# Performance work log

Measured on AMD Instinct MI355X. Metric: run time of the kernel, lower is better.

The kernel has to match this reference:

```python
import jax, jax.numpy as jnp
import numpy as np

N_ROWS = 262144
FEAT = 1024
N_CORES = 4096
SEG = N_ROWS // N_CORES
H1 = H2 = H3 = 1024
NUM_CLASSES = 2
BN_EPS = 1e-5


def setup_inputs() -> dict:
    key = jax.random.key(0)
    ks = jax.random.split(key, 12)
    x = jax.random.normal(ks[0], (N_ROWS, FEAT), dtype=jnp.float32)
    # equal-length segments: start indices 0, SEG, 2*SEG, ...
    corelen = (jnp.arange(N_CORES) * SEG).astype(jnp.int64)
    def lin(k, din, dout):
        kw, kb = jax.random.split(k)
        W = jax.random.normal(kw, (din, dout), dtype=jnp.float32) / np.sqrt(din)
        b = jnp.zeros((dout,), dtype=jnp.float32)
        return W, b
    W1, b1 = lin(ks[1], FEAT, H1)
    W2, b2 = lin(ks[2], H1, H2)
    W3, b3 = lin(ks[3], H2, H3)
    W4, b4 = lin(ks[4], H3, NUM_CLASSES)
    g1 = jnp.ones((H1,), jnp.float32); be1 = jnp.zeros((H1,), jnp.float32)
    g2 = jnp.ones((H2,), jnp.float32); be2 = jnp.zeros((H2,), jnp.float32)
    g3 = jnp.ones((H3,), jnp.float32); be3 = jnp.zeros((H3,), jnp.float32)
    return {"x": x, "corelen": corelen,
            "W1": W1, "b1": b1, "g1": g1, "be1": be1,
            "W2": W2, "b2": b2, "g2": g2, "be2": be2,
            "W3": W3, "b3": b3, "g3": g3, "be3": be3,
            "W4": W4, "b4": b4}


def _batchnorm(h, g, b):
    # BatchNorm1d, training mode: biased batch statistics over the batch dim
    m = jnp.mean(h, axis=0)
    v = jnp.mean(jnp.square(h - m), axis=0)
    return g * (h - m) * jax.lax.rsqrt(v + BN_EPS) + b


def reference(x, corelen, W1, b1, g1, be1, W2, b2, g2, be2, W3, b3, g3, be3, W4, b4):
    n = x.shape[0]
    # segment id of row r = number of starts <= r, minus 1 (rows before
    # corelen[0] get id -1 and are dropped, matching the torch loop)
    seg_ids = jnp.searchsorted(corelen, jnp.arange(n), side="right") - 1
    agg = jax.ops.segment_sum(x, seg_ids, num_segments=corelen.shape[0])  # [C, FEAT]
    h = jax.nn.relu(_batchnorm(agg @ W1 + b1, g1, be1))
    h = jax.nn.relu(_batchnorm(h @ W2 + b2, g2, be2))
    h = jax.nn.relu(_batchnorm(h @ W3 + b3, g3, be3))
    return h @ W4 + b4  # [C, NUM_CLASSES]
```

## Files before the change

### kernel.cpp

```cpp
#include <hip/hip_runtime.h>
#include <hip/hip_bf16.h>
#include <stdint.h>

#define N_ROWS 262144
#define FEAT 1024
#define N_CORES 4096
#define HDIM 1024
#define BN_EPS 1e-5f

typedef __attribute__((ext_vector_type(8))) short bf16x8;
typedef __attribute__((ext_vector_type(8))) unsigned short u16x8;
typedef __attribute__((ext_vector_type(4))) float f32x4;

__device__ __forceinline__ unsigned short f2bf(float f) {
  __hip_bfloat16 h = __float2bfloat16(f);
  return __builtin_bit_cast(unsigned short, h);
}
__device__ __forceinline__ float bf2f(unsigned short u) {
  unsigned int x = ((unsigned int)u) << 16;
  return __builtin_bit_cast(float, x);
}

__device__ __forceinline__ void gll16(const unsigned short* g, unsigned short* l) {
  __builtin_amdgcn_global_load_lds(
      (const __attribute__((address_space(1))) void*)g,
      (__attribute__((address_space(3))) void*)l, 16, 0, 0);
}

__global__ __launch_bounds__(256)
void k_prep(const float* __restrict__ x, const int* __restrict__ corelen,
            unsigned short* __restrict__ aggb,
            const float* __restrict__ W1, const float* __restrict__ W2,
            const float* __restrict__ W3, unsigned short* __restrict__ Wt,
            float* __restrict__ stats) {
  const int bid = blockIdx.x;
  const int t = threadIdx.x;
  if (bid < N_CORES) {
    const int seg = bid;
    const int start = corelen[seg];
    const int end = (seg + 1 < N_CORES) ? corelen[seg + 1] : N_ROWS;
    f32x4 a0 = {0.f, 0.f, 0.f, 0.f};
    f32x4 a1 = {0.f, 0.f, 0.f, 0.f};
    f32x4 a2 = {0.f, 0.f, 0.f, 0.f};
    f32x4 a3 = {0.f, 0.f, 0.f, 0.f};
    const f32x4* xp = (const f32x4*)(x + (size_t)start * FEAT) + t;
    int r = start;
    for (; r + 4 <= end; r += 4) {
      const f32x4 v0 = __builtin_nontemporal_load(xp);
      const f32x4 v1 = __builtin_nontemporal_load(xp + 256);
      const f32x4 v2 = __builtin_nontemporal_load(xp + 512);
      const f32x4 v3 = __builtin_nontemporal_load(xp + 768);
      a0 += v0; a1 += v1; a2 += v2; a3 += v3;
      xp += 4 * 256;
    }
    for (; r < end; ++r) {
      a0 += *xp;
      xp += 256;
    }
    a0 += a1; a2 += a3; a0 += a2;
    ushort4 o;
    o.x = f2bf(a0.x); o.y = f2bf(a0.y); o.z = f2bf(a0.z); o.w = f2bf(a0.w);
    *(ushort4*)(aggb + (size_t)seg * FEAT + t * 4) = o;
  } else if (bid < N_CORES + 3 * 1024) {
    __shared__ unsigned short tile[32][33];
    const int id = bid - N_CORES;
    const int l = id >> 10;
    const int q = id & 1023;
    const int n0 = (q & 31) * 32;
    const int k0 = (q >> 5) * 32;
    const float* W = (l == 0) ? W1 : (l == 1) ? W2 : W3;
    unsigned short* Wo = Wt + (size_t)l * HDIM * HDIM;
    const int tx = t & 31, ty = t >> 5;
#pragma unroll
    for (int i = 0; i < 4; ++i)
      tile[ty + 8 * i][tx] = f2bf(W[(size_t)(k0 + ty + 8 * i) * HDIM + n0 + tx]);
    __syncthreads();
#pragma unroll
    for (int i = 0; i < 4; ++i)
      Wo[(size_t)(n0 + ty + 8 * i) * HDIM + k0 + tx] = tile[tx][ty + 8 * i];
  } else {
#pragma unroll
    for (int i = 0; i < 24; ++i) stats[t + i * 256] = 0.f;
  }
}

#define BM 64
#define BN 64
#define BK 64
#define NT (HDIM / BK)
__global__ __launch_bounds__(64)
void k_gemm_bt(const unsigned short* __restrict__ A,
               const unsigned short* __restrict__ Bt,
               const float* __restrict__ bias,
               unsigned short* __restrict__ C,
               float* __restrict__ sums, float* __restrict__ sumsq) {
  __shared__ unsigned short As[2][BM * BK];
  __shared__ unsigned short Bs[2][BN * BK];
  const int lane = threadIdx.x;
  const int tileM = blockIdx.x * BM;
  const int tileN = blockIdx.y * BN;
  const int fr = lane & 15;
  const int kk = (lane >> 4) * 8;
  const int lr = lane >> 3;
  const int sc = ((lane & 7) * 8) ^ (lr << 3);

  const unsigned short* pA = A + (size_t)(tileM + lr) * HDIM + sc;
  const unsigned short* pB = Bt + (size_t)(tileN + lr) * HDIM + sc;

  f32x4 acc[4][4] = {};

#define STAGE(buf, k0)                                                     \
  do {                                                                     \
    _Pragma("unroll") for (int j = 0; j < 8; ++j)                          \
        gll16(pA + (k0) + j * 8 * HDIM, &As[buf][(j * 8) * BK]);           \
    _Pragma("unroll") for (int j = 0; j < 8; ++j)                          \
        gll16(pB + (k0) + j * 8 * HDIM, &Bs[buf][(j * 8) * BK]);           \
  } while (0)

  STAGE(0, 0);
  STAGE(1, BK);
  for (int kt = 0; kt < NT; ++kt) {
    const int cur = kt & 1;
    if (kt < NT - 1)
      asm volatile("s_waitcnt vmcnt(16)" ::: "memory");
    else
      asm volatile("s_waitcnt vmcnt(0)" ::: "memory");
    __builtin_amdgcn_sched_barrier(0);
    bf16x8 af[2][4], bfv[2][4];
#pragma unroll
    for (int ks = 0; ks < 2; ++ks) {
      const int pc = (ks * 32 + kk) ^ ((fr & 7) << 3);
#pragma unroll
      for (int m = 0; m < 4; ++m)
        af[ks][m] = *(const bf16x8*)&As[cur][(m * 16 + fr) * BK + pc];
#pragma unroll
      for (int n = 0; n < 4; ++n)
        bfv[ks][n] = *(const bf16x8*)&Bs[cur][(n * 16 + fr) * BK + pc];
    }
    asm volatile("s_waitcnt lgkmcnt(0)" ::: "memory");
    __builtin_amdgcn_sched_barrier(0);
    if (kt + 2 < NT) STAGE(cur, (kt + 2) * BK);
#pragma unroll
    for (int ks = 0; ks < 2; ++ks)
#pragma unroll
      for (int m = 0; m < 4; ++m)
#pragma unroll
        for (int n = 0; n < 4; ++n)
          acc[m][n] = __builtin_amdgcn_mfma_f32_16x16x32_bf16(
              af[ks][m], bfv[ks][n], acc[m][n], 0, 0, 0);
  }
#undef STAGE

  const int cr = (lane >> 4) * 4;
  const int cc = lane & 15;
#pragma unroll
  for (int n = 0; n < 4; ++n) {
    const int col = tileN + n * 16 + cc;
    const float bv = bias[col];
    float s = 0.f, s2 = 0.f;
#pragma unroll
    for (int m = 0; m < 4; ++m) {
      unsigned short* cp = C + (size_t)(tileM + m * 16 + cr) * HDIM + col;
#pragma unroll
      for (int j = 0; j < 4; ++j) {
        const float h = acc[m][n][j] + bv;
        cp[(size_t)j * HDIM] = f2bf(h);
        s += h; s2 += h * h;
      }
    }
    s  += __shfl_xor(s, 16, 64);  s  += __shfl_xor(s, 32, 64);
    s2 += __shfl_xor(s2, 16, 64); s2 += __shfl_xor(s2, 32, 64);
    if ((lane >> 4) == 0) {
      atomicAdd(&sums[col], s);
      atomicAdd(&sumsq[col], s2);
    }
  }
}

__global__ __launch_bounds__(256)
void k_norm_relu(const unsigned short* __restrict__ Hb,
                 const float* __restrict__ sums, const float* __restrict__ sumsq,
                 const float* __restrict__ g, const float* __restrict__ be,
                 unsigned short* __restrict__ Ab) {
  const size_t i8 = ((size_t)blockIdx.x * 256 + threadIdx.x) * 8;
  const u16x8 v = *(const u16x8*)(Hb + i8);
  const int c = (int)(i8 & (HDIM - 1));
  u16x8 o;
#pragma unroll
  for (int j = 0; j < 8; ++j) {
    const float mean = sums[c + j] * (1.f / N_CORES);
    const float var = sumsq[c + j] * (1.f / N_CORES) - mean * mean;
    const float sc = g[c + j] * rsqrtf(var + BN_EPS);
    const float sh = be[c + j] - mean * sc;
    o[j] = f2bf(fmaxf(bf2f(v[j]) * sc + sh, 0.f));
  }
  *(u16x8*)(Ab + i8) = o;
}

__global__ __launch_bounds__(256)
void k_final(const unsigned short* __restrict__ Hb,
             const float* __restrict__ sums, const float* __restrict__ sumsq,
             const float* __restrict__ g, const float* __restrict__ be,
             const float* __restrict__ W4, const float* __restrict__ b4,
             float* __restrict__ out) {
  const int t = threadIdx.x;
  const int w = t >> 6, lane = t & 63;
  const int row = blockIdx.x * 4 + w;
  const int kbase = lane * 16;
  const unsigned short* a = Hb + (size_t)row * HDIM + kbase;
  float s0 = 0.f, s1 = 0.f;
#pragma unroll
  for (int j = 0; j < 16; ++j) {
    const int col = kbase + j;
    const float mean = sums[col] * (1.f / N_CORES);
    const float var = sumsq[col] * (1.f / N_CORES) - mean * mean;
    const float sc = g[col] * rsqrtf(var + BN_EPS);
    const float sh = be[col] - mean * sc;
    const float av = fmaxf(bf2f(a[j]) * sc + sh, 0.f);
    s0 += av * W4[col * 2 + 0];
    s1 += av * W4[col * 2 + 1];
  }
#pragma unroll
  for (int off = 32; off >= 1; off >>= 1) {
    s0 += __shfl_down(s0, off, 64);
    s1 += __shfl_down(s1, off, 64);
  }
  if (lane == 0) {
    out[row * 2 + 0] = s0 + b4[0];
    out[row * 2 + 1] = s1 + b4[1];
  }
}

extern "C" void kernel_launch(void* const* d_in, const int* in_sizes, int n_in,
                              void* d_out, int out_size, void* d_ws, size_t ws_size,
                              hipStream_t stream) {
  (void)in_sizes; (void)n_in; (void)out_size; (void)ws_size;
  const float* x       = (const float*)d_in[0];
  const int* corelen   = (const int*)d_in[1];
  const float* W1  = (const float*)d_in[2];
  const float* b1  = (const float*)d_in[3];
  const float* g1  = (const float*)d_in[4];
  const float* be1 = (const float*)d_in[5];
  const float* W2  = (const float*)d_in[6];
  const float* b2  = (const float*)d_in[7];
  const float* g2  = (const float*)d_in[8];
  const float* be2 = (const float*)d_in[9];
  const float* W3  = (const float*)d_in[10];
  const float* b3  = (const float*)d_in[11];
  const float* g3  = (const float*)d_in[12];
  const float* be3 = (const float*)d_in[13];
  const float* W4  = (const float*)d_in[14];
  const float* b4  = (const float*)d_in[15];
  float* out = (float*)d_out;

  char* ws = (char*)d_ws;
  unsigned short* Hb   = (unsigned short*)(ws);
  unsigned short* Abf  = (unsigned short*)(ws + (8u << 20));
  unsigned short* Wt   = (unsigned short*)(ws + (16u << 20));
  float* stats = (float*)(ws + (22u << 20));

  k_prep<<<N_CORES + 3 * 1024 + 1, 256, 0, stream>>>(
      x, corelen, Abf, W1, W2, W3, Wt, stats);

  const float* bs[3]  = {b1, b2, b3};
  const float* gs[3]  = {g1, g2, g3};
  const float* bes[3] = {be1, be2, be3};
  for (int l = 0; l < 3; ++l) {
    float* sums  = stats + l * 2 * HDIM;
    float* sumsq = sums + HDIM;
    k_gemm_bt<<<dim3(N_CORES / BM, HDIM / BN), 64, 0, stream>>>(
        Abf, Wt + (size_t)l * HDIM * HDIM, bs[l], Hb, sums, sumsq);
    if (l < 2)
      k_norm_relu<<<(N_CORES * HDIM / 8) / 256, 256, 0, stream>>>(
          Hb, sums, sumsq, gs[l], bes[l], Abf);
    else
      k_final<<<N_CORES / 4, 256, 0, stream>>>(
          Hb, sums, sumsq, gs[l], bes[l], W4, b4, out);
  }
}
```

Baseline: 249.8 us.

## Fuse batchnorm+relu and final projection into GEMM via cooperative grid sync

Each layer becomes one cooperative kernel. It runs the GEMM, accumulates the column statistics, waits on a grid-wide barrier, then applies batchnorm and ReLU straight from registers and writes the next activation. The final layer folds the 1024x2 projection into the epilogue with atomics into an output pre-seeded with the bias. This removes the bf16 intermediate round-trip and the separate norm and final kernels. It relies on all 1024 blocks being co-resident and adds the cost of a grid sync plus output atomics.

```diff
diff --git a/kernel.cpp b/kernel.cpp
--- a/kernel.cpp
+++ b/kernel.cpp
@@ -1,6 +1,9 @@
 #include <hip/hip_runtime.h>
 #include <hip/hip_bf16.h>
+#include <hip/hip_cooperative_groups.h>
 #include <stdint.h>
+
+namespace cg = cooperative_groups;
 
 #define N_ROWS 262144
 #define FEAT 1024
@@ -9,16 +12,11 @@
 #define BN_EPS 1e-5f
 
 typedef __attribute__((ext_vector_type(8))) short bf16x8;
-typedef __attribute__((ext_vector_type(8))) unsigned short u16x8;
 typedef __attribute__((ext_vector_type(4))) float f32x4;
 
 __device__ __forceinline__ unsigned short f2bf(float f) {
   __hip_bfloat16 h = __float2bfloat16(f);
   return __builtin_bit_cast(unsigned short, h);
-}
-__device__ __forceinline__ float bf2f(unsigned short u) {
-  unsigned int x = ((unsigned int)u) << 16;
-  return __builtin_bit_cast(float, x);
 }
 
 __device__ __forceinline__ void gll16(const unsigned short* g, unsigned short* l) {
@@ -32,7 +30,8 @@
             unsigned short* __restrict__ aggb,
             const float* __restrict__ W1, const float* __restrict__ W2,
             const float* __restrict__ W3, unsigned short* __restrict__ Wt,
-            float* __restrict__ stats) {
+            float* __restrict__ stats, float* __restrict__ out,
+            const float* __restrict__ b4) {
   const int bid = blockIdx.x;
   const int t = threadIdx.x;
   if (bid < N_CORES) {
@@ -81,6 +80,12 @@
   } else {
 #pragma unroll
     for (int i = 0; i < 24; ++i) stats[t + i * 256] = 0.f;
+    const float bv0 = b4[0], bv1 = b4[1];
+#pragma unroll
+    for (int i = 0; i < 32; ++i) {
+      const int idx = t + i * 256;
+      out[idx] = (idx & 1) ? bv1 : bv0;
+    }
   }
 }
 
@@ -89,16 +94,20 @@
 #define BK 64
 #define NT (HDIM / BK)
 __global__ __launch_bounds__(64)
-void k_gemm_bt(const unsigned short* __restrict__ A,
-               const unsigned short* __restrict__ Bt,
-               const float* __restrict__ bias,
-               unsigned short* __restrict__ C,
-               float* __restrict__ sums, float* __restrict__ sumsq) {
+void k_layer(const unsigned short* __restrict__ A,
+             const unsigned short* __restrict__ Bt,
+             const float* __restrict__ bias,
+             const float* __restrict__ g, const float* __restrict__ be,
+             float* __restrict__ sums, float* __restrict__ sumsq,
+             unsigned short* __restrict__ Aout,
+             const float* __restrict__ W4, float* __restrict__ out,
+             int is_final) {
   __shared__ unsigned short As[2][BM * BK];
   __shared__ unsigned short Bs[2][BN * BK];
   const int lane = threadIdx.x;
-  const int tileM = blockIdx.x * BM;
-  const int tileN = blockIdx.y * BN;
+  const int bid = blockIdx.x;
+  const int tileM = (bid & 63) * BM;
+  const int tileN = (bid >> 6) * BN;
   const int fr = lane & 15;
   const int kk = (lane >> 4) * 8;
   const int lr = lane >> 3;
@@ -153,21 +162,19 @@
 
   const int cr = (lane >> 4) * 4;
   const int cc = lane & 15;
+  float bv[4];
 #pragma unroll
   for (int n = 0; n < 4; ++n) {
     const int col = tileN + n * 16 + cc;
-    const float bv = bias[col];
+    bv[n] = bias[col];
     float s = 0.f, s2 = 0.f;
 #pragma unroll
-    for (int m = 0; m < 4; ++m) {
-      unsigned short* cp = C + (size_t)(tileM + m * 16 + cr) * HDIM + col;
+    for (int m = 0; m < 4; ++m)
 #pragma unroll
       for (int j = 0; j < 4; ++j) {
-        const float h = acc[m][n][j] + bv;
-        cp[(size_t)j * HDIM] = f2bf(h);
+        const float h = acc[m][n][j] + bv[n];
         s += h; s2 += h * h;
       }
-    }
     s  += __shfl_xor(s, 16, 64);  s  += __shfl_xor(s, 32, 64);
     s2 += __shfl_xor(s2, 16, 64); s2 += __shfl_xor(s2, 32, 64);
     if ((lane >> 4) == 0) {
@@ -175,59 +182,65 @@
       atomicAdd(&sumsq[col], s2);
     }
   }
-}
-
-__global__ __launch_bounds__(256)
-void k_norm_relu(const unsigned short* __restrict__ Hb,
-                 const float* __restrict__ sums, const float* __restrict__ sumsq,
-                 const float* __restrict__ g, const float* __restrict__ be,
-                 unsigned short* __restrict__ Ab) {
-  const size_t i8 = ((size_t)blockIdx.x * 256 + threadIdx.x) * 8;
-  const u16x8 v = *(const u16x8*)(Hb + i8);
-  const int c = (int)(i8 & (HDIM - 1));
-  u16x8 o;
-#pragma unroll
-  for (int j = 0; j < 8; ++j) {
-    const float mean = sums[c + j] * (1.f / N_CORES);
-    const float var = sumsq[c + j] * (1.f / N_CORES) - mean * mean;
-    const float sc = g[c + j] * rsqrtf(var + BN_EPS);
-    const float sh = be[c + j] - mean * sc;
-    o[j] = f2bf(fmaxf(bf2f(v[j]) * sc + sh, 0.f));
-  }
-  *(u16x8*)(Ab + i8) = o;
-}
-
-__global__ __launch_bounds__(256)
-void k_final(const unsigned short* __restrict__ Hb,
-             const float* __restrict__ sums, const float* __restrict__ sumsq,
-             const float* __restrict__ g, const float* __restrict__ be,
-             const float* __restrict__ W4, const float* __restrict__ b4,
-             float* __restrict__ out) {
-  const int t = threadIdx.x;
-  const int w = t >> 6, lane = t & 63;
-  const int row = blockIdx.x * 4 + w;
-  const int kbase = lane * 16;
-  const unsigned short* a = Hb + (size_t)row * HDIM + kbase;
-  float s0 = 0.f, s1 = 0.f;
-#pragma unroll
-  for (int j = 0; j < 16; ++j) {
-    const int col = kbase + j;
+
+  __threadfence();
+  cg::this_grid().sync();
+
+  float scl[4], shf[4];
+#pragma unroll
+  for (int n = 0; n < 4; ++n) {
+    const int col = tileN + n * 16 + cc;
     const float mean = sums[col] * (1.f / N_CORES);
     const float var = sumsq[col] * (1.f / N_CORES) - mean * mean;
-    const float sc = g[col] * rsqrtf(var + BN_EPS);
-    const float sh = be[col] - mean * sc;
-    const float av = fmaxf(bf2f(a[j]) * sc + sh, 0.f);
-    s0 += av * W4[col * 2 + 0];
-    s1 += av * W4[col * 2 + 1];
-  }
-#pragma unroll
-  for (int off = 32; off >= 1; off >>= 1) {
-    s0 += __shfl_down(s0, off, 64);
-    s1 += __shfl_down(s1, off, 64);
-  }
-  if (lane == 0) {
-    out[row * 2 + 0] = s0 + b4[0];
-    out[row * 2 + 1] = s1 + b4[1];
+    const float scv = g[col] * rsqrtf(var + BN_EPS);
+    scl[n] = scv;
+    shf[n] = be[col] - mean * scv;
+  }
+
+  if (!is_final) {
+#pragma unroll
+    for (int n = 0; n < 4; ++n) {
+      const int col = tileN + n * 16 + cc;
+      unsigned short* cp = Aout + (size_t)(tileM + cr) * HDIM + col;
+#pragma unroll
+      for (int m = 0; m < 4; ++m)
+#pragma unroll
+        for (int j = 0; j < 4; ++j) {
+          const float h = acc[m][n][j] + bv[n];
+          cp[(size_t)(m * 16 + j) * HDIM] = f2bf(fmaxf(h * scl[n] + shf[n], 0.f));
+        }
+    }
+  } else {
+    float w0[4], w1[4];
+#pragma unroll
+    for (int n = 0; n < 4; ++n) {
+      const int col = tileN + n * 16 + cc;
+      w0[n] = W4[col * 2 + 0];
+      w1[n] = W4[col * 2 + 1];
+    }
+#pragma unroll
+    for (int m = 0; m < 4; ++m)
+#pragma unroll
+      for (int j = 0; j < 4; ++j) {
+        float s0 = 0.f, s1 = 0.f;
+#pragma unroll
+        for (int n = 0; n < 4; ++n) {
+          const float h = acc[m][n][j] + bv[n];
+          const float a = fmaxf(h * scl[n] + shf[n], 0.f);
+          s0 += a * w0[n];
+          s1 += a * w1[n];
+        }
+#pragma unroll
+        for (int off = 1; off < 16; off <<= 1) {
+          s0 += __shfl_xor(s0, off, 64);
+          s1 += __shfl_xor(s1, off, 64);
+        }
+        if ((lane & 15) == 0) {
+          const int row = tileM + m * 16 + cr + j;
+          atomicAdd(&out[row * 2 + 0], s0);
+          atomicAdd(&out[row * 2 + 1], s1);
+        }
+      }
   }
 }
 
@@ -254,27 +267,33 @@
   float* out = (float*)d_out;
 
   char* ws = (char*)d_ws;
-  unsigned short* Hb   = (unsigned short*)(ws);
-  unsigned short* Abf  = (unsigned short*)(ws + (8u << 20));
+  unsigned short* Act0 = (unsigned short*)(ws);
+  unsigned short* Act1 = (unsigned short*)(ws + (8u << 20));
   unsigned short* Wt   = (unsigned short*)(ws + (16u << 20));
   float* stats = (float*)(ws + (22u << 20));
 
   k_prep<<<N_CORES + 3 * 1024 + 1, 256, 0, stream>>>(
-      x, corelen, Abf, W1, W2, W3, Wt, stats);
+      x, corelen, Act0, W1, W2, W3, Wt, stats, out, b4);
 
   const float* bs[3]  = {b1, b2, b3};
   const float* gs[3]  = {g1, g2, g3};
   const float* bes[3] = {be1, be2, be3};
+  unsigned short* ain[3]  = {Act0, Act1, Act0};
+  unsigned short* aout[3] = {Act1, Act0, Act1};
   for (int l = 0; l < 3; ++l) {
+    const unsigned short* A = ain[l];
+    const unsigned short* B = Wt + (size_t)l * HDIM * HDIM;
+    const float* bias = bs[l];
+    const float* g = gs[l];
+    const float* be = bes[l];
     float* sums  = stats + l * 2 * HDIM;
     float* sumsq = sums + HDIM;
-    k_gemm_bt<<<dim3(N_CORES / BM, HDIM / BN), 64, 0, stream>>>(
-        Abf, Wt + (size_t)l * HDIM * HDIM, bs[l], Hb, sums, sumsq);
-    if (l < 2)
-      k_norm_relu<<<(N_CORES * HDIM / 8) / 256, 256, 0, stream>>>(
-          Hb, sums, sumsq, gs[l], bes[l], Abf);
-    else
-      k_final<<<N_CORES / 4, 256, 0, stream>>>(
-          Hb, sums, sumsq, gs[l], bes[l], W4, b4, out);
-  }
-}
+    unsigned short* Ao = aout[l];
+    int is_final = (l == 2);
+    void* args[] = {(void*)&A, (void*)&B, (void*)&bias, (void*)&g, (void*)&be,
+                    (void*)&sums, (void*)&sumsq, (void*)&Ao, (void*)&W4,
+                    (void*)&out, (void*)&is_final};
+    hipLaunchCooperativeKernel((void*)k_layer, dim3(1024), dim3(64), args, 0,
+                               stream);
+  }
+}
```

After: 644.3 us. 158% more time.
